# Optimization experiments

Measured on AMD Instinct MI355X. Metric: run time of the kernel, lower is better.

The kernel has to match this reference:

```python
import jax, jax.numpy as jnp
import numpy as np

N_KERNELS = 5
MUL_FACTOR = 2.0


def setup_inputs() -> dict:
    key = jax.random.key(0)
    X = jax.random.normal(key, (4096, 64), dtype=jnp.float32)
    # bandwidth multipliers: mul_factor ** (arange(K) - K//2)
    bandwidth_multipliers = (MUL_FACTOR ** (jnp.arange(N_KERNELS) - N_KERNELS // 2)).astype(jnp.float32)
    return {"X": X, "bandwidth_multipliers": bandwidth_multipliers}


def reference(X, bandwidth_multipliers):
    # squared pairwise euclidean distances: ||x_i||^2 + ||x_j||^2 - 2 x_i . x_j
    sq_norms = jnp.sum(X * X, axis=-1)                      # [N]
    gram = X @ X.T                                          # [N, N]
    L2 = jnp.maximum(sq_norms[:, None] + sq_norms[None, :] - 2.0 * gram, 0.0)  # [N, N]

    # bandwidth estimate uses .data in torch -> stop_gradient
    n = X.shape[0]
    bw = jax.lax.stop_gradient(L2.sum()) / (n * n - n)

    # sum over K bandwidth-scaled RBF kernels
    scales = bw * bandwidth_multipliers                     # [K]
    out = jnp.sum(jnp.exp(-L2[None, :, :] / scales[:, None, None]), axis=0)  # [N, N]
    return out
```

## Files before the change

kernel.cpp:

```cpp
#include <hip/hip_runtime.h>
#include <hip/hip_bf16.h>
#include <math.h>

#define N 4096
#define TILE 128
#define PB 128

typedef __attribute__((ext_vector_type(8))) short short8;
typedef __attribute__((ext_vector_type(4))) float floatx4;


__device__ inline unsigned bfpk(float a, float b) {
    unsigned ua = __float_as_uint(a), ub = __float_as_uint(b);
    ua = (ua + 0x7fffu + ((ua >> 16) & 1u)) >> 16;
    ub = (ub + 0x7fffu + ((ub >> 16) & 1u)) >> 16;
    return ua | (ub << 16);
}

__device__ inline uint4 pack8(float4 f0, float4 f1) {
    uint4 r;
    r.x = bfpk(f0.x, f0.y);
    r.y = bfpk(f0.z, f0.w);
    r.z = bfpk(f1.x, f1.y);
    r.w = bfpk(f1.z, f1.w);
    return r;
}

__global__ __launch_bounds__(256) void prep_kernel(const float* __restrict__ X,
                                                   float* __restrict__ ws) {
    __shared__ float sm[256];
    __shared__ float ssum[4];
    const int lane = threadIdx.x & 63, w = threadIdx.x >> 6;
    const int b = blockIdx.x;
    const int row0 = (b * 4 + w) * 8;
    float mloc = 0.f, Sloc = 0.f;
    #pragma unroll
    for (int rr = 0; rr < 8; ++rr) {
        float x = X[(size_t)(row0 + rr) * 64 + lane];
        mloc += x; Sloc += x * x;
    }
    sm[threadIdx.x] = mloc;
    #pragma unroll
    for (int off = 1; off < 64; off <<= 1) Sloc += __shfl_xor(Sloc, off, 64);
    if (lane == 0) ssum[w] = Sloc;
    __syncthreads();
    if (threadIdx.x < 64) {
        ws[b * 66 + threadIdx.x] =
            sm[threadIdx.x] + sm[64 + threadIdx.x] + sm[128 + threadIdx.x] + sm[192 + threadIdx.x];
    } else if (threadIdx.x == 64) {
        ws[b * 66 + 64] = ssum[0] + ssum[1] + ssum[2] + ssum[3];
    }
}

__global__ __launch_bounds__(256, 4) void rbf_kernel(const float* __restrict__ X,
                                                     const float* __restrict__ ws,
                                                     float* __restrict__ out) {
    __shared__ uint4 lA[1024];
    __shared__ uint4 lB[1024];
    __shared__ float sR[128];
    __shared__ float sC[128];

    const int t  = threadIdx.x;
    const int rowBase = blockIdx.y * TILE, colBase = blockIdx.x * TILE;

    #pragma unroll
    for (int i = 0; i < 4; ++i) {
        int slot = i * 256 + t;
        int r = slot >> 3;
        int g = slot & 7;
        int c = g ^ (r & 7);
        const float4* pa = (const float4*)(X + (size_t)(rowBase + r) * 64 + c * 8);
        float4 a0 = pa[0], a1 = pa[1];
        lA[slot] = pack8(a0, a1);
        float na = a0.x*a0.x + a0.y*a0.y + a0.z*a0.z + a0.w*a0.w
                 + a1.x*a1.x + a1.y*a1.y + a1.z*a1.z + a1.w*a1.w;
        const float4* pb = (const float4*)(X + (size_t)(colBase + r) * 64 + c * 8);
        float4 b0 = pb[0], b1 = pb[1];
        lB[slot] = pack8(b0, b1);
        float nb = b0.x*b0.x + b0.y*b0.y + b0.z*b0.z + b0.w*b0.w
                 + b1.x*b1.x + b1.y*b1.y + b1.z*b1.z + b1.w*b1.w;
        #pragma unroll
        for (int off = 1; off < 8; off <<= 1) {
            na += __shfl_xor(na, off, 64);
            nb += __shfl_xor(nb, off, 64);
        }
        if (g == 0) { sR[r] = na; sC[r] = nb; }
    }

    const int lane = t & 63;
    float mv = 0.f;
    #pragma unroll 8
    for (int b = 0; b < PB; ++b) mv += ws[b * 66 + lane];
    float Sv = ws[lane * 66 + 64] + ws[(lane + 64) * 66 + 64];
    float mm = mv * mv;
    #pragma unroll
    for (int off = 1; off < 64; off <<= 1) {
        mm += __shfl_xor(mm, off, 64);
        Sv += __shfl_xor(Sv, off, 64);
    }
    float sumL2 = 2.0f * (float)N * Sv - 2.0f * mm;
    const float c1 = -1.4426950408889634f * (float)(N * N - N) / sumL2;

    __syncthreads();

    const int wave = t >> 6;
    const int wr = (wave >> 1) * 64;
    const int wc = (wave & 1) * 64;
    const int lr = lane & 15, q = lane >> 4;

    short8 a[4][2];
    #pragma unroll
    for (int ti = 0; ti < 4; ++ti) {
        #pragma unroll
        for (int ks = 0; ks < 2; ++ks) {
            int c = ks * 4 + q;
            int r1 = wr + ti * 16 + lr;
            a[ti][ks] = *reinterpret_cast<const short8*>(&lA[8 * r1 + (c ^ (r1 & 7))]);
        }
    }

    floatx4 acc[4][4];
    #pragma unroll
    for (int ti = 0; ti < 4; ++ti)
        #pragma unroll
        for (int tj = 0; tj < 4; ++tj)
            acc[ti][tj] = (floatx4){0.f, 0.f, 0.f, 0.f};

    #pragma unroll
    for (int tj = 0; tj < 4; ++tj) {
        int r2 = wc + tj * 16 + lr;
        short8 b0 = *reinterpret_cast<const short8*>(&lB[8 * r2 + ((q    ) ^ (r2 & 7))]);
        short8 b1 = *reinterpret_cast<const short8*>(&lB[8 * r2 + ((q + 4) ^ (r2 & 7))]);
        #pragma unroll
        for (int ti = 0; ti < 4; ++ti) {
            acc[ti][tj] = __builtin_amdgcn_mfma_f32_16x16x32_bf16(a[ti][0], b0, acc[ti][tj], 0, 0, 0);
            acc[ti][tj] = __builtin_amdgcn_mfma_f32_16x16x32_bf16(a[ti][1], b1, acc[ti][tj], 0, 0, 0);
        }
    }

    #pragma unroll
    for (int ti = 0; ti < 4; ++ti) {
        int rb = wr + ti * 16 + q * 4;
        #pragma unroll
        for (int tj = 0; tj < 4; ++tj) {
            int cl = wc + tj * 16 + lr;
            float scj = sC[cl];
            size_t col = (size_t)(colBase + cl);
            #pragma unroll
            for (int p = 0; p < 4; ++p) {
                int rl = rb + p;
                float d2 = sR[rl] + scj - 2.0f * acc[ti][tj][p];
                d2 = fmaxf(d2, 0.0f);
                float e  = __builtin_amdgcn_exp2f(d2 * c1);
                float e2 = e * e;
                float e4 = e2 * e2;
                float s1 = __builtin_amdgcn_sqrtf(e);
                float s2 = __builtin_amdgcn_sqrtf(s1);
                out[(size_t)(rowBase + rl) * N + col] = e4 + e2 + e + s1 + s2;
            }
        }
    }
}

extern "C" void kernel_launch(void* const* d_in, const int* in_sizes, int n_in,
                              void* d_out, int out_size, void* d_ws, size_t ws_size,
                              hipStream_t stream) {
    const float* X = (const float*)d_in[0];
    float* out = (float*)d_out;
    float* ws  = (float*)d_ws;

    prep_kernel<<<PB, 256, 0, stream>>>(X, ws);
    rbf_kernel<<<dim3(N / TILE, N / TILE), 256, 0, stream>>>(X, ws, out);
}
```

Measured before the change: 91.39 us.

## Exploit output symmetry with triangular tile schedule and transposed stores

Launches only the upper-triangular 128x128 tiles, each split into two 64-row halves, and writes each computed tile both normally and transposed as float4 stores, about halving the MFMA and exp work. The multi-scale exponentials are now built from one exp2 of a quarter-scaled argument followed by repeated squaring, which removes the two sqrt calls. The prep kernel also uses fewer blocks, each reducing more rows. The transposed float4 stores are strided across rows, so the write pattern is less coalesced. Squaring also changes rounding slightly.

```diff
diff --git a/kernel.cpp b/kernel.cpp
--- a/kernel.cpp
+++ b/kernel.cpp
@@ -3,8 +3,7 @@
 #include <math.h>
 
 #define N 4096
-#define TILE 128
-#define PB 128
+#define PB 32
 
 typedef __attribute__((ext_vector_type(8))) short short8;
 typedef __attribute__((ext_vector_type(4))) float floatx4;
@@ -32,10 +31,10 @@
     __shared__ float ssum[4];
     const int lane = threadIdx.x & 63, w = threadIdx.x >> 6;
     const int b = blockIdx.x;
-    const int row0 = (b * 4 + w) * 8;
+    const int row0 = b * 128 + w * 32;
     float mloc = 0.f, Sloc = 0.f;
     #pragma unroll
-    for (int rr = 0; rr < 8; ++rr) {
+    for (int rr = 0; rr < 32; ++rr) {
         float x = X[(size_t)(row0 + rr) * 64 + lane];
         mloc += x; Sloc += x * x;
     }
@@ -52,46 +51,66 @@
     }
 }
 
-__global__ __launch_bounds__(256, 4) void rbf_kernel(const float* __restrict__ X,
-                                                     const float* __restrict__ ws,
-                                                     float* __restrict__ out) {
-    __shared__ uint4 lA[1024];
+__global__ __launch_bounds__(256) void rbf_kernel(const float* __restrict__ X,
+                                                  const float* __restrict__ ws,
+                                                  float* __restrict__ out) {
+    __shared__ uint4 lA[512];
     __shared__ uint4 lB[1024];
-    __shared__ float sR[128];
+    __shared__ float sR[64];
     __shared__ float sC[128];
 
-    const int t  = threadIdx.x;
-    const int rowBase = blockIdx.y * TILE, colBase = blockIdx.x * TILE;
+    const int t_ = threadIdx.x;
+    const int b  = blockIdx.x;
+
+    int I, J, h;
+    if (b < 64) {
+        I = J = b >> 1; h = b & 1;
+    } else {
+        int t = (b - 64) >> 1; h = (b - 64) & 1;
+        int i = (int)((63.0f - sqrtf((float)(3969 - 8 * t))) * 0.5f);
+        while (31 * (i + 1) - ((i + 1) * i) / 2 <= t) ++i;
+        while (31 * i - (i * (i - 1)) / 2 > t) --i;
+        int oi = 31 * i - (i * (i - 1)) / 2;
+        I = i; J = i + 1 + (t - oi);
+    }
+    const int rowBase = I * 128 + h * 64;
+    const int colBase = J * 128;
+    const bool offdiag = (I != J);
 
     #pragma unroll
     for (int i = 0; i < 4; ++i) {
-        int slot = i * 256 + t;
-        int r = slot >> 3;
-        int g = slot & 7;
+        int slot = i * 256 + t_;
+        int r = slot >> 3, g = slot & 7;
         int c = g ^ (r & 7);
-        const float4* pa = (const float4*)(X + (size_t)(rowBase + r) * 64 + c * 8);
-        float4 a0 = pa[0], a1 = pa[1];
-        lA[slot] = pack8(a0, a1);
-        float na = a0.x*a0.x + a0.y*a0.y + a0.z*a0.z + a0.w*a0.w
-                 + a1.x*a1.x + a1.y*a1.y + a1.z*a1.z + a1.w*a1.w;
-        const float4* pb = (const float4*)(X + (size_t)(colBase + r) * 64 + c * 8);
-        float4 b0 = pb[0], b1 = pb[1];
-        lB[slot] = pack8(b0, b1);
-        float nb = b0.x*b0.x + b0.y*b0.y + b0.z*b0.z + b0.w*b0.w
-                 + b1.x*b1.x + b1.y*b1.y + b1.z*b1.z + b1.w*b1.w;
+        const float4* p = (const float4*)(X + (size_t)(colBase + r) * 64 + c * 8);
+        float4 f0 = p[0], f1 = p[1];
+        lB[slot] = pack8(f0, f1);
+        float nb = f0.x*f0.x + f0.y*f0.y + f0.z*f0.z + f0.w*f0.w
+                 + f1.x*f1.x + f1.y*f1.y + f1.z*f1.z + f1.w*f1.w;
         #pragma unroll
-        for (int off = 1; off < 8; off <<= 1) {
-            na += __shfl_xor(na, off, 64);
-            nb += __shfl_xor(nb, off, 64);
-        }
-        if (g == 0) { sR[r] = na; sC[r] = nb; }
+        for (int off = 1; off < 8; off <<= 1) nb += __shfl_xor(nb, off, 64);
+        if (g == 0) sC[r] = nb;
+    }
+    #pragma unroll
+    for (int i = 0; i < 2; ++i) {
+        int slot = i * 256 + t_;
+        int r = slot >> 3, g = slot & 7;
+        int c = g ^ (r & 7);
+        const float4* p = (const float4*)(X + (size_t)(rowBase + r) * 64 + c * 8);
+        float4 f0 = p[0], f1 = p[1];
+        lA[slot] = pack8(f0, f1);
+        float na = f0.x*f0.x + f0.y*f0.y + f0.z*f0.z + f0.w*f0.w
+                 + f1.x*f1.x + f1.y*f1.y + f1.z*f1.z + f1.w*f1.w;
+        #pragma unroll
+        for (int off = 1; off < 8; off <<= 1) na += __shfl_xor(na, off, 64);
+        if (g == 0) sR[r] = na;
     }
 
-    const int lane = t & 63;
+    const int lane = t_ & 63;
     float mv = 0.f;
     #pragma unroll 8
-    for (int b = 0; b < PB; ++b) mv += ws[b * 66 + lane];
-    float Sv = ws[lane * 66 + 64] + ws[(lane + 64) * 66 + 64];
+    for (int pb = 0; pb < PB; ++pb) mv += ws[pb * 66 + lane];
+    float Sv = (lane < PB) ? ws[lane * 66 + 64] : 0.f;
     float mm = mv * mv;
     #pragma unroll
     for (int off = 1; off < 64; off <<= 1) {
@@ -99,65 +118,54 @@
         Sv += __shfl_xor(Sv, off, 64);
     }
     float sumL2 = 2.0f * (float)N * Sv - 2.0f * mm;
-    const float c1 = -1.4426950408889634f * (float)(N * N - N) / sumL2;
+    const float c1q = -1.4426950408889634f * 0.25f * (float)((size_t)N * N - N) / sumL2;
 
     __syncthreads();
 
-    const int wave = t >> 6;
-    const int wr = (wave >> 1) * 64;
-    const int wc = (wave & 1) * 64;
+    const int wave = t_ >> 6;
     const int lr = lane & 15, q = lane >> 4;
 
-    short8 a[4][2];
+    int r1 = wave * 16 + lr;
+    short8 a0 = *reinterpret_cast<const short8*>(&lA[8 * r1 + ((q    ) ^ (r1 & 7))]);
+    short8 a1 = *reinterpret_cast<const short8*>(&lA[8 * r1 + ((q + 4) ^ (r1 & 7))]);
+
+    floatx4 acc[8];
     #pragma unroll
-    for (int ti = 0; ti < 4; ++ti) {
-        #pragma unroll
-        for (int ks = 0; ks < 2; ++ks) {
-            int c = ks * 4 + q;
-            int r1 = wr + ti * 16 + lr;
-            a[ti][ks] = *reinterpret_cast<const short8*>(&lA[8 * r1 + (c ^ (r1 & 7))]);
-        }
+    for (int tj = 0; tj < 8; ++tj) acc[tj] = (floatx4){0.f, 0.f, 0.f, 0.f};
+
+    #pragma unroll
+    for (int tj = 0; tj < 8; ++tj) {
+        int r2 = tj * 16 + lr;
+        short8 b0 = *reinterpret_cast<const short8*>(&lB[8 * r2 + ((q    ) ^ (r2 & 7))]);
+        short8 b1 = *reinterpret_cast<const short8*>(&lB[8 * r2 + ((q + 4) ^ (r2 & 7))]);
+        acc[tj] = __builtin_amdgcn_mfma_f32_16x16x32_bf16(a0, b0, acc[tj], 0, 0, 0);
+        acc[tj] = __builtin_amdgcn_mfma_f32_16x16x32_bf16(a1, b1, acc[tj], 0, 0, 0);
     }
 
-    floatx4 acc[4][4];
+    const int rb = wave * 16 + q * 4;
+    float sr0 = sR[rb], sr1 = sR[rb + 1], sr2 = sR[rb + 2], sr3 = sR[rb + 3];
     #pragma unroll
-    for (int ti = 0; ti < 4; ++ti)
+    for (int tj = 0; tj < 8; ++tj) {
+        int cl = tj * 16 + lr;
+        float scj = sC[cl];
+        size_t col = (size_t)(colBase + cl);
+        float4 tp;
         #pragma unroll
-        for (int tj = 0; tj < 4; ++tj)
-            acc[ti][tj] = (floatx4){0.f, 0.f, 0.f, 0.f};
-
-    #pragma unroll
-    for (int tj = 0; tj < 4; ++tj) {
-        int r2 = wc + tj * 16 + lr;
-        short8 b0 = *reinterpret_cast<const short8*>(&lB[8 * r2 + ((q    ) ^ (r2 & 7))]);
-        short8 b1 = *reinterpret_cast<const short8*>(&lB[8 * r2 + ((q + 4) ^ (r2 & 7))]);
-        #pragma unroll
-        for (int ti = 0; ti < 4; ++ti) {
-            acc[ti][tj] = __builtin_amdgcn_mfma_f32_16x16x32_bf16(a[ti][0], b0, acc[ti][tj], 0, 0, 0);
-            acc[ti][tj] = __builtin_amdgcn_mfma_f32_16x16x32_bf16(a[ti][1], b1, acc[ti][tj], 0, 0, 0);
+        for (int p = 0; p < 4; ++p) {
+            float srp = (p == 0) ? sr0 : (p == 1) ? sr1 : (p == 2) ? sr2 : sr3;
+            float d2 = srp + scj - 2.0f * acc[tj][p];
+            d2 = fmaxf(d2, 0.0f);
+            float u  = __builtin_amdgcn_exp2f(d2 * c1q);
+            float s1 = u * u;
+            float e  = s1 * s1;
+            float e2 = e * e;
+            float e4 = e2 * e2;
+            float val = e4 + e2 + e + s1 + u;
+            out[(size_t)(rowBase + rb + p) * N + col] = val;
+            ((float*)&tp)[p] = val;
         }
-    }
-
-    #pragma unroll
-    for (int ti = 0; ti < 4; ++ti) {
-        int rb = wr + ti * 16 + q * 4;
-        #pragma unroll
-        for (int tj = 0; tj < 4; ++tj) {
-            int cl = wc + tj * 16 + lr;
-            float scj = sC[cl];
-            size_t col = (size_t)(colBase + cl);
-            #pragma unroll
-            for (int p = 0; p < 4; ++p) {
-                int rl = rb + p;
-                float d2 = sR[rl] + scj - 2.0f * acc[ti][tj][p];
-                d2 = fmaxf(d2, 0.0f);
-                float e  = __builtin_amdgcn_exp2f(d2 * c1);
-                float e2 = e * e;
-                float e4 = e2 * e2;
-                float s1 = __builtin_amdgcn_sqrtf(e);
-                float s2 = __builtin_amdgcn_sqrtf(s1);
-                out[(size_t)(rowBase + rl) * N + col] = e4 + e2 + e + s1 + s2;
-            }
+        if (offdiag) {
+            *reinterpret_cast<float4*>(&out[col * (size_t)N + (rowBase + rb)]) = tp;
         }
     }
 }
@@ -170,5 +178,5 @@
     float* ws  = (float*)d_ws;
 
     prep_kernel<<<PB, 256, 0, stream>>>(X, ws);
-    rbf_kernel<<<dim3(N / TILE, N / TILE), 256, 0, stream>>>(X, ws, out);
+    rbf_kernel<<<1056, 256, 0, stream>>>(X, ws, out);
 }
```

After: 85.57 us. 6.4% less time.
